# Performance work log

Measured on AMD Instinct MI355X. Metric: run time of the kernel, lower is better.

The kernel has to match this reference:

```python
import jax, jax.numpy as jnp
import numpy as np

TEMP = 11.313708498984761  # sqrt(head_dim=128)

def setup_inputs() -> dict:
    key = jax.random.key(0)
    kq, kk, kv, km = jax.random.split(key, 4)
    B, H, S, D = 2, 16, 2048, 128
    q = jax.random.normal(kq, (B, H, S, D), dtype=jnp.float32)
    k = jax.random.normal(kk, (B, H, S, D), dtype=jnp.float32)
    v = jax.random.normal(kv, (B, H, S, D), dtype=jnp.float32)
    mask = jax.random.randint(km, (B, 1, S, S), 0, 2, dtype=jnp.int32)
    return {"q": q, "k": k, "v": v, "mask": mask}

def reference(q, k, v, mask):
    # atten = (q / temp) @ k^T  -> [B,H,S,S]
    atten = jnp.einsum("bhsd,bhtd->bhst", q / TEMP, k)
    maskf = mask.astype(atten.dtype)
    # torch masked_fill_(mask.bool(), 1e-9): positions where mask != 0 get 1e-9
    atten = jnp.where(mask.astype(bool), jnp.asarray(1e-9, atten.dtype), atten)
    atten = jax.nn.softmax(atten, axis=-1)
    # then multiply by mask (zeros out mask==0 positions)
    atten = atten * maskf
    # dropout: eval mode (identity) for a deterministic correctness baseline
    out = jnp.einsum("bhst,bhtd->bhsd", atten, v)
    return (out, atten)
```

## Files before the change

kernel.cpp:

```cpp
#include <hip/hip_runtime.h>
#include <stdint.h>

#define B_ 2
#define H_ 16
#define S_ 2048
#define D_ 128

typedef float f32x4 __attribute__((ext_vector_type(4)));
typedef float f32x16 __attribute__((ext_vector_type(16)));
typedef short bf16x8 __attribute__((ext_vector_type(8)));
typedef unsigned short u16x4 __attribute__((ext_vector_type(4)));
typedef int i32x4 __attribute__((ext_vector_type(4)));

__device__ __forceinline__ unsigned short f2bf(float x){
  union { float f; uint32_t u; } c; c.f = x;
  uint32_t u = c.u;
  uint32_t r = (u + 0x7FFFu + ((u >> 16) & 1u)) >> 16;
  return (unsigned short)r;
}

__device__ __forceinline__ void gload_lds16(const void* g, void* l){
  __builtin_amdgcn_global_load_lds(
      (const __attribute__((address_space(1))) unsigned int*)g,
      (__attribute__((address_space(3))) unsigned int*)l, 16, 0, 0);
}

__global__ void kconv_kernel(const float* __restrict__ k, unsigned short* __restrict__ KB){
  size_t i = (size_t)blockIdx.x * 256 + threadIdx.x;
  f32x4 v = __builtin_nontemporal_load(&((const f32x4*)k)[i]);
  u16x4 o; o[0]=f2bf(v.x); o[1]=f2bf(v.y); o[2]=f2bf(v.z); o[3]=f2bf(v.w);
  __builtin_nontemporal_store(o, &((u16x4*)KB)[i]);
}

__global__ void vtrans_kernel(const float* __restrict__ v, unsigned short* __restrict__ VT){
  __shared__ float tile[64][73];
  int blk = blockIdx.x;
  int bh = blk >> 6;
  int ts = (blk >> 1) & 31;
  int dsec = blk & 1;
  int t0 = ts*64, d0 = dsec*64;
  const float* vb = v + ((size_t)bh*S_ + t0)*D_ + d0;
  int tid = threadIdx.x;
  #pragma unroll
  for (int i=0;i<4;++i){
    int fi = i*256 + tid;
    int r = fi >> 4;
    int c4 = (fi & 15) * 4;
    f32x4 val = __builtin_nontemporal_load((const f32x4*)(vb + (size_t)r*D_ + c4));
    tile[r][c4+0]=val.x; tile[r][c4+1]=val.y; tile[r][c4+2]=val.z; tile[r][c4+3]=val.w;
  }
  __syncthreads();
  unsigned short* ob = VT + ((size_t)bh*D_ + d0)*S_ + t0;
  #pragma unroll
  for (int i=0;i<4;++i){
    int ui = i*256 + tid;
    int dr = ui >> 4;
    int tc = (ui & 15) * 4;
    u16x4 o;
    o[0] = f2bf(tile[tc+0][dr]);
    o[1] = f2bf(tile[tc+1][dr]);
    o[2] = f2bf(tile[tc+2][dr]);
    o[3] = f2bf(tile[tc+3][dr]);
    __builtin_nontemporal_store(o, (u16x4*)(ob + (size_t)dr*S_ + tc));
  }
}

__global__ void maskprep_kernel(const int* __restrict__ mask, unsigned long long* __restrict__ bits){
  int row = blockIdx.x;
  const int* mrow = mask + (size_t)row*S_;
  int w = threadIdx.x >> 6;
  int lane = threadIdx.x & 63;
  #pragma unroll
  for (int i=0;i<8;++i){
    int t = i*256 + threadIdx.x;
    unsigned long long bm = __ballot(__builtin_nontemporal_load(&mrow[t]) != 0);
    if (lane == 0) bits[(size_t)row*32 + i*4 + w] = bm;
  }
}

__launch_bounds__(512, 4)
__global__ void fused_kernel(const float* __restrict__ q,
                             const unsigned long long* __restrict__ bits,
                             const unsigned short* __restrict__ KB,
                             const unsigned short* __restrict__ VT,
                             float* __restrict__ outp,
                             float* __restrict__ c_ws)
{
  __shared__ __align__(16) unsigned char Ksm[2][16384];
  __shared__ __align__(16) unsigned char Vsm[2][16384];
  __shared__ float lred[8][32];
  const int tid = threadIdx.x;
  const int lane = tid & 63;
  const int w = tid >> 6;
  const int l32 = lane & 31;
  const int lh = lane >> 5;

  const int orig = blockIdx.x;
  const int blk = (orig & 7) * 64 + (orig >> 3);
  const int bh = blk >> 4;
  const int qt = blk & 15;
  const int b = bh >> 4;
  const int s0 = qt * 128;
  const int r = w >> 1;
  const int cQ = w & 1;
  const int qrow = s0 + 32*r + l32;

  const float QS = 1.4426950408889634f / 11.313708498984761f;

  bf16x8 qf[8];
  {
    const float* qp = q + ((size_t)bh*S_ + qrow)*D_ + 8*lh;
    #pragma unroll
    for (int m=0; m<8; ++m){
      f32x4 a0 = __builtin_nontemporal_load((const f32x4*)(qp + 16*m));
      f32x4 a1 = __builtin_nontemporal_load((const f32x4*)(qp + 16*m + 4));
      bf16x8 f;
      f[0]=(short)f2bf(a0.x*QS); f[1]=(short)f2bf(a0.y*QS);
      f[2]=(short)f2bf(a0.z*QS); f[3]=(short)f2bf(a0.w*QS);
      f[4]=(short)f2bf(a1.x*QS); f[5]=(short)f2bf(a1.y*QS);
      f[6]=(short)f2bf(a1.z*QS); f[7]=(short)f2bf(a1.w*QS);
      qf[m] = f;
    }
  }

  f32x16 Wacc[2];
  #pragma unroll
  for (int n=0;n<2;++n)
    #pragma unroll
    for (int e=0;e<16;++e) Wacc[n][e] = 0.f;
  float lsum = 0.f;

  const unsigned char* Kgb = (const unsigned char*)(KB + (size_t)bh*S_*D_);
  const unsigned char* Vgb = (const unsigned char*)(VT + (size_t)bh*D_*S_);
  const unsigned long long* bitsb = bits + (size_t)b*S_*32 + (size_t)qrow*32;

  uint32_t koff[2], voff[2];
  int kbase[2];
  {
    int lq = lane >> 4, ls = lane & 15;
    #pragma unroll
    for (int i=0;i<2;++i){
      int c = 2*w + i;
      kbase[i] = c*1024;
      int rr = c*4 + lq;
      int ss = ls ^ (rr & 15);
      koff[i] = (uint32_t)(rr*256 + ss*16);
      int d  = rr*2 + (ss>>3);
      int ts = ss & 7;
      voff[i] = (uint32_t)(d*(S_*2) + ts*16);
    }
  }

  unsigned long long mbn = bitsb[0];
  #pragma unroll
  for (int i=0;i<2;++i){
    gload_lds16(Kgb + koff[i], &Ksm[0][kbase[i]]);
    gload_lds16(Vgb + voff[i], &Vsm[0][kbase[i]]);
  }

  int cur = 0;
  for (int it=0; it<32; ++it){
    asm volatile("s_waitcnt vmcnt(0)" ::: "memory");
    __builtin_amdgcn_sched_barrier(0);
    __builtin_amdgcn_s_barrier();
    __builtin_amdgcn_sched_barrier(0);

    unsigned long long mb = mbn;
    if (it+1 < 32){
      mbn = bitsb[it+1];
      const unsigned char* Kp = Kgb + (size_t)(it+1)*16384;
      const unsigned char* Vp = Vgb + (size_t)(it+1)*128;
      #pragma unroll
      for (int i=0;i<2;++i){
        gload_lds16(Kp + koff[i], &Ksm[cur^1][kbase[i]]);
        gload_lds16(Vp + voff[i], &Vsm[cur^1][kbase[i]]);
      }
      __builtin_amdgcn_sched_barrier(0);
    }

    f32x16 Sacc;
    #pragma unroll
    for (int e=0;e<16;++e) Sacc[e] = 0.f;
    const int trow = 32*cQ + l32;
    const unsigned char* kb = &Ksm[cur][trow*256];
    const int txr = trow & 15;
    __builtin_amdgcn_s_setprio(1);
    #pragma unroll
    for (int m=0; m<8; ++m){
      int slot = (2*m + lh) ^ txr;
      bf16x8 kf = *(const bf16x8*)(kb + (slot<<4));
      Sacc = __builtin_amdgcn_mfma_f32_32x32x16_bf16(kf, qf[m], Sacc, 0,0,0);
    }
    __builtin_amdgcn_s_setprio(0);

    uint32_t mw = (uint32_t)(mb >> (32*cQ + 4*lh));
    #pragma unroll
    for (int reg=0; reg<16; ++reg){
      const int tb = (reg&3) + 8*(reg>>2);
      float x = ((mw >> tb) & 1u) ? 0.f : Sacc[reg];
      lsum += __builtin_amdgcn_exp2f(x);
    }

    unsigned long long ms = mb >> (8*lh);
    uint32_t mlo = (uint32_t)ms, mhi = (uint32_t)(ms >> 32);
    #pragma unroll
    for (int m2=0; m2<4; ++m2){
      uint32_t bt = ((m2 < 2 ? mlo : mhi) >> (16*(m2&1))) & 0xFFu;
      union { bf16x8 v; uint32_t u[4]; } pk;
      #pragma unroll
      for (int j2=0; j2<4; ++j2){
        pk.u[j2] = (((bt>>(2*j2))&1u) ? 0x3F80u : 0u)
                 | (((bt>>(2*j2+1))&1u) ? 0x3F800000u : 0u);
      }
      __builtin_amdgcn_s_setprio(1);
      #pragma unroll
      for (int n=0; n<2; ++n){
        const int dd = 32*(2*cQ + n) + l32;
        int slot = ((((dd&1)<<3) | (2*m2 + lh)) ^ ((dd>>1)&15));
        bf16x8 vf = *(const bf16x8*)(&Vsm[cur][(dd>>1)*256 + (slot<<4)]);
        Wacc[n] = __builtin_amdgcn_mfma_f32_32x32x16_bf16(pk.v, vf, Wacc[n], 0,0,0);
      }
      __builtin_amdgcn_s_setprio(0);
    }
    cur ^= 1;
  }

  lsum += __shfl_xor(lsum, 32);
  if (lane < 32) lred[w][l32] = lsum;
  __syncthreads();

  if (tid < 128){
    int rr = tid >> 5;
    float cc = 1.0f / (lred[2*rr][tid&31] + lred[2*rr+1][tid&31]);
    c_ws[(size_t)bh*S_ + s0 + tid] = cc;
  }
  #pragma unroll
  for (int reg=0; reg<16; ++reg){
    int crow = (reg&3) + 8*(reg>>2) + 4*lh;
    float cv = 1.0f / (lred[2*r][crow] + lred[2*r+1][crow]);
    int row = s0 + 32*r + crow;
    #pragma unroll
    for (int n=0; n<2; ++n){
      const int dd = 32*(2*cQ + n) + l32;
      __builtin_nontemporal_store(cv*Wacc[n][reg],
                                  &outp[((size_t)bh*S_ + row)*D_ + dd]);
    }
  }
}

__global__ void atten_kernel(const unsigned long long* __restrict__ bits,
                             const float* __restrict__ c_ws,
                             float* __restrict__ atten){
  int blk = blockIdx.x;
  int bq = blk >> 11;
  int s  = blk & 2047;
  __shared__ float csm[16];
  if (threadIdx.x < 16)
    csm[threadIdx.x] = c_ws[((size_t)(bq*H_ + threadIdx.x))*S_ + s];
  __syncthreads();
  const unsigned long long* wrow = bits + ((size_t)bq*S_ + s)*32;
  for (int i = threadIdx.x; i < S_/4; i += 256){
    unsigned long long wv = wrow[i >> 4];
    uint32_t nib = (uint32_t)(wv >> ((i & 15)*4)) & 0xFu;
    #pragma unroll
    for (int h=0; h<H_; ++h){
      float c = csm[h];
      f32x4 o = { (nib&1u)?c:0.f, (nib&2u)?c:0.f, (nib&4u)?c:0.f, (nib&8u)?c:0.f };
      __builtin_nontemporal_store(o, ((f32x4*)(atten + (((size_t)(bq*H_ + h)*S_ + s)*S_))) + i);
    }
  }
}

extern "C" void kernel_launch(void* const* d_in, const int* in_sizes, int n_in,
                              void* d_out, int out_size, void* d_ws, size_t ws_size,
                              hipStream_t stream){
  const float* q = (const float*)d_in[0];
  const float* k = (const float*)d_in[1];
  const float* v = (const float*)d_in[2];
  const int* mask = (const int*)d_in[3];
  float* outp = (float*)d_out;
  float* atten = outp + (size_t)B_*H_*S_*D_;

  unsigned short* KB = (unsigned short*)d_ws;
  unsigned short* VT = KB + (size_t)B_*H_*S_*D_;
  float* c_ws = (float*)(VT + (size_t)B_*H_*S_*D_);
  unsigned long long* bits = (unsigned long long*)(c_ws + (size_t)B_*H_*S_);

  hipLaunchKernelGGL(maskprep_kernel, dim3(4096), dim3(256), 0, stream, mask, bits);
  hipLaunchKernelGGL(kconv_kernel,  dim3(8192), dim3(256), 0, stream, k, KB);
  hipLaunchKernelGGL(vtrans_kernel, dim3(2048), dim3(256), 0, stream, v, VT);
  hipLaunchKernelGGL(fused_kernel,  dim3(512),  dim3(512), 0, stream, q, bits, KB, VT, outp, c_ws);
  hipLaunchKernelGGL(atten_kernel,  dim3(4096), dim3(256), 0, stream, bits, c_ws, atten);
}
```

Baseline: 262.8 us.

## Fuse attention-matrix write into fused kernel epilogue and merge prep kernels

The separate atten kernel is removed: each attention block now loads its mask bits and row normalizers into shared memory and writes its 128 rows of the attention matrix directly. The three prep kernels (K convert, V transpose, mask bit-packing) are merged into one launch via block-index ranges. This removes the normalizer workspace round-trip and two launches, and lets the large atten writes overlap with other blocks' compute. The risk is that each block's long store tail lowers overlap or occupancy compared with a dedicated bandwidth-bound kernel.

```diff
diff --git a/kernel.cpp b/kernel.cpp
--- a/kernel.cpp
+++ b/kernel.cpp
@@ -25,56 +25,58 @@
       (__attribute__((address_space(3))) unsigned int*)l, 16, 0, 0);
 }
 
-__global__ void kconv_kernel(const float* __restrict__ k, unsigned short* __restrict__ KB){
-  size_t i = (size_t)blockIdx.x * 256 + threadIdx.x;
-  f32x4 v = __builtin_nontemporal_load(&((const f32x4*)k)[i]);
-  u16x4 o; o[0]=f2bf(v.x); o[1]=f2bf(v.y); o[2]=f2bf(v.z); o[3]=f2bf(v.w);
-  __builtin_nontemporal_store(o, &((u16x4*)KB)[i]);
-}
-
-__global__ void vtrans_kernel(const float* __restrict__ v, unsigned short* __restrict__ VT){
+__global__ void prep_kernel(const float* __restrict__ k, const float* __restrict__ v,
+                            const int* __restrict__ mask,
+                            unsigned short* __restrict__ KB, unsigned short* __restrict__ VT,
+                            unsigned long long* __restrict__ bits){
   __shared__ float tile[64][73];
-  int blk = blockIdx.x;
-  int bh = blk >> 6;
-  int ts = (blk >> 1) & 31;
-  int dsec = blk & 1;
-  int t0 = ts*64, d0 = dsec*64;
-  const float* vb = v + ((size_t)bh*S_ + t0)*D_ + d0;
-  int tid = threadIdx.x;
-  #pragma unroll
-  for (int i=0;i<4;++i){
-    int fi = i*256 + tid;
-    int r = fi >> 4;
-    int c4 = (fi & 15) * 4;
-    f32x4 val = __builtin_nontemporal_load((const f32x4*)(vb + (size_t)r*D_ + c4));
-    tile[r][c4+0]=val.x; tile[r][c4+1]=val.y; tile[r][c4+2]=val.z; tile[r][c4+3]=val.w;
-  }
-  __syncthreads();
-  unsigned short* ob = VT + ((size_t)bh*D_ + d0)*S_ + t0;
-  #pragma unroll
-  for (int i=0;i<4;++i){
-    int ui = i*256 + tid;
-    int dr = ui >> 4;
-    int tc = (ui & 15) * 4;
-    u16x4 o;
-    o[0] = f2bf(tile[tc+0][dr]);
-    o[1] = f2bf(tile[tc+1][dr]);
-    o[2] = f2bf(tile[tc+2][dr]);
-    o[3] = f2bf(tile[tc+3][dr]);
-    __builtin_nontemporal_store(o, (u16x4*)(ob + (size_t)dr*S_ + tc));
-  }
-}
-
-__global__ void maskprep_kernel(const int* __restrict__ mask, unsigned long long* __restrict__ bits){
-  int row = blockIdx.x;
-  const int* mrow = mask + (size_t)row*S_;
-  int w = threadIdx.x >> 6;
-  int lane = threadIdx.x & 63;
-  #pragma unroll
-  for (int i=0;i<8;++i){
-    int t = i*256 + threadIdx.x;
-    unsigned long long bm = __ballot(__builtin_nontemporal_load(&mrow[t]) != 0);
-    if (lane == 0) bits[(size_t)row*32 + i*4 + w] = bm;
+  const int blk = blockIdx.x;
+  const int tid = threadIdx.x;
+  if (blk < 8192){
+    size_t i = (size_t)blk * 256 + tid;
+    f32x4 val = __builtin_nontemporal_load(&((const f32x4*)k)[i]);
+    u16x4 o; o[0]=f2bf(val.x); o[1]=f2bf(val.y); o[2]=f2bf(val.z); o[3]=f2bf(val.w);
+    __builtin_nontemporal_store(o, &((u16x4*)KB)[i]);
+  } else if (blk < 10240){
+    int b2 = blk - 8192;
+    int bh = b2 >> 6;
+    int ts = (b2 >> 1) & 31;
+    int dsec = b2 & 1;
+    int t0 = ts*64, d0 = dsec*64;
+    const float* vb = v + ((size_t)bh*S_ + t0)*D_ + d0;
+    #pragma unroll
+    for (int i=0;i<4;++i){
+      int fi = i*256 + tid;
+      int r = fi >> 4;
+      int c4 = (fi & 15) * 4;
+      f32x4 val = __builtin_nontemporal_load((const f32x4*)(vb + (size_t)r*D_ + c4));
+      tile[r][c4+0]=val.x; tile[r][c4+1]=val.y; tile[r][c4+2]=val.z; tile[r][c4+3]=val.w;
+    }
+    __syncthreads();
+    unsigned short* ob = VT + ((size_t)bh*D_ + d0)*S_ + t0;
+    #pragma unroll
+    for (int i=0;i<4;++i){
+      int ui = i*256 + tid;
+      int dr = ui >> 4;
+      int tc = (ui & 15) * 4;
+      u16x4 o;
+      o[0] = f2bf(tile[tc+0][dr]);
+      o[1] = f2bf(tile[tc+1][dr]);
+      o[2] = f2bf(tile[tc+2][dr]);
+      o[3] = f2bf(tile[tc+3][dr]);
+      __builtin_nontemporal_store(o, (u16x4*)(ob + (size_t)dr*S_ + tc));
+    }
+  } else {
+    int row = blk - 10240;
+    const int* mrow = mask + (size_t)row*S_;
+    int w = tid >> 6;
+    int lane = tid & 63;
+    #pragma unroll
+    for (int i=0;i<8;++i){
+      int t = i*256 + tid;
+      unsigned long long bm = __ballot(__builtin_nontemporal_load(&mrow[t]) != 0);
+      if (lane == 0) bits[(size_t)row*32 + i*4 + w] = bm;
+    }
   }
 }
 
@@ -84,7 +86,7 @@
                              const unsigned short* __restrict__ KB,
                              const unsigned short* __restrict__ VT,
                              float* __restrict__ outp,
-                             float* __restrict__ c_ws)
+                             float* __restrict__ atten)
 {
   __shared__ __align__(16) unsigned char Ksm[2][16384];
   __shared__ __align__(16) unsigned char Vsm[2][16384];
@@ -229,11 +231,20 @@
   if (lane < 32) lred[w][l32] = lsum;
   __syncthreads();
 
-  if (tid < 128){
-    int rr = tid >> 5;
-    float cc = 1.0f / (lred[2*rr][tid&31] + lred[2*rr+1][tid&31]);
-    c_ws[(size_t)bh*S_ + s0 + tid] = cc;
-  }
+  unsigned long long* bitlds = (unsigned long long*)&Ksm[0][0];
+  float* csm = (float*)&Vsm[0][0];
+  {
+    const i32x4* bsrc = (const i32x4*)(bits + ((size_t)b*S_ + s0)*32);
+    i32x4* bdst = (i32x4*)bitlds;
+    #pragma unroll
+    for (int i=0;i<4;++i)
+      bdst[i*512 + tid] = bsrc[i*512 + tid];
+    if (tid < 128){
+      int rr = tid >> 5;
+      csm[tid] = 1.0f / (lred[2*rr][tid&31] + lred[2*rr+1][tid&31]);
+    }
+  }
+
   #pragma unroll
   for (int reg=0; reg<16; ++reg){
     int crow = (reg&3) + 8*(reg>>2) + 4*lh;
@@ -246,27 +257,19 @@
                                   &outp[((size_t)bh*S_ + row)*D_ + dd]);
     }
   }
-}
-
-__global__ void atten_kernel(const unsigned long long* __restrict__ bits,
-                             const float* __restrict__ c_ws,
-                             float* __restrict__ atten){
-  int blk = blockIdx.x;
-  int bq = blk >> 11;
-  int s  = blk & 2047;
-  __shared__ float csm[16];
-  if (threadIdx.x < 16)
-    csm[threadIdx.x] = c_ws[((size_t)(bq*H_ + threadIdx.x))*S_ + s];
+
   __syncthreads();
-  const unsigned long long* wrow = bits + ((size_t)bq*S_ + s)*32;
-  for (int i = threadIdx.x; i < S_/4; i += 256){
-    unsigned long long wv = wrow[i >> 4];
-    uint32_t nib = (uint32_t)(wv >> ((i & 15)*4)) & 0xFu;
-    #pragma unroll
-    for (int h=0; h<H_; ++h){
-      float c = csm[h];
+
+  {
+    f32x4* abase = (f32x4*)(atten + ((size_t)bh*S_ + s0)*S_);
+    const int word = tid >> 4;
+    const int sh = (tid & 15)*4;
+    for (int j=0; j<128; ++j){
+      float c = csm[j];
+      unsigned long long wv = bitlds[j*32 + word];
+      uint32_t nib = (uint32_t)(wv >> sh) & 0xFu;
       f32x4 o = { (nib&1u)?c:0.f, (nib&2u)?c:0.f, (nib&4u)?c:0.f, (nib&8u)?c:0.f };
-      __builtin_nontemporal_store(o, ((f32x4*)(atten + (((size_t)(bq*H_ + h)*S_ + s)*S_))) + i);
+      __builtin_nontemporal_store(o, &abase[j*512 + tid]);
     }
   }
 }
@@ -283,12 +286,8 @@
 
   unsigned short* KB = (unsigned short*)d_ws;
   unsigned short* VT = KB + (size_t)B_*H_*S_*D_;
-  float* c_ws = (float*)(VT + (size_t)B_*H_*S_*D_);
-  unsigned long long* bits = (unsigned long long*)(c_ws + (size_t)B_*H_*S_);
-
-  hipLaunchKernelGGL(maskprep_kernel, dim3(4096), dim3(256), 0, stream, mask, bits);
-  hipLaunchKernelGGL(kconv_kernel,  dim3(8192), dim3(256), 0, stream, k, KB);
-  hipLaunchKernelGGL(vtrans_kernel, dim3(2048), dim3(256), 0, stream, v, VT);
-  hipLaunchKernelGGL(fused_kernel,  dim3(512),  dim3(512), 0, stream, q, bits, KB, VT, outp, c_ws);
-  hipLaunchKernelGGL(atten_kernel,  dim3(4096), dim3(256), 0, stream, bits, c_ws, atten);
-}
+  unsigned long long* bits = (unsigned long long*)(VT + (size_t)B_*H_*S_*D_);
+
+  hipLaunchKernelGGL(prep_kernel,  dim3(14336), dim3(256), 0, stream, k, v, mask, KB, VT, bits);
+  hipLaunchKernelGGL(fused_kernel, dim3(512),   dim3(512), 0, stream, q, bits, KB, VT, outp, atten);
+}
```

Result: faster. 223.1 us, median of 3 (-15.1%).
